# Optimization experiments

Measured on AMD Instinct MI355X. Metric: run time of the kernel, lower is better.

Reference implementation:

```python
import jax, jax.numpy as jnp
import numpy as np
from jax import lax

B, N, C_IN = 8, 16384, 32
NPOINT = 1024
RADII = (0.5, 1.0)
NSAMPLES = (16, 32)
MLPS = ((35, 32, 64), (35, 64, 128))  # first dim includes +3 for use_xyz


def setup_inputs():
    key = jax.random.key(0)
    ks = jax.random.split(key, 20)
    inp = {
        'xyz': jax.random.normal(ks[0], (B, N, 3), jnp.float32),
        'features': jax.random.normal(ks[1], (B, C_IN, N), jnp.float32),
    }
    i = 2
    for bi, spec in enumerate(MLPS):
        for li in range(len(spec) - 1):
            cin, cout = spec[li], spec[li + 1]
            inp['w%d_%d' % (bi, li)] = jax.random.normal(ks[i], (cout, cin), jnp.float32) * np.float32(1.0 / np.sqrt(cin)); i += 1
            inp['s%d_%d' % (bi, li)] = jax.random.uniform(ks[i], (cout,), jnp.float32, minval=0.5, maxval=1.5); i += 1
            inp['b%d_%d' % (bi, li)] = jax.random.normal(ks[i], (cout,), jnp.float32) * 0.1; i += 1
    return inp


def _fps(xyz, npoint):
    # iterative D-FPS, start from index 0 (matches CUDA furthest_point_sampling)
    Bb, Nn, _ = xyz.shape
    def body(carry, _):
        dists, far = carry
        centroid = jnp.take_along_axis(xyz, far[:, None, None], axis=1)  # (B,1,3)
        d = jnp.sum((xyz - centroid) ** 2, axis=-1)                       # (B,N)
        dists = jnp.minimum(dists, d)
        return (dists, jnp.argmax(dists, axis=-1).astype(jnp.int32)), far
    init = (jnp.full((Bb, Nn), 1e10, jnp.float32), jnp.zeros((Bb,), jnp.int32))
    _, idx = lax.scan(body, init, None, length=npoint)
    return idx.T  # (B, npoint)


def _ball_query(dist2, radius, nsample):
    # first-nsample-in-index-order semantics of pointnet2 ball_query;
    # empty slots padded with first hit (0 if no hit at all)
    Nn = dist2.shape[-1]
    scores = jnp.where(dist2 < radius * radius, jnp.arange(Nn, dtype=jnp.int32), Nn)
    neg, _ = lax.top_k(-scores, nsample)  # nsample smallest indices
    idx = -neg
    first = jnp.where(idx[..., :1] == Nn, 0, idx[..., :1])
    return jnp.where(idx == Nn, first, idx)


def _forward(xyz, features, params):
    fwx = jnp.concatenate([xyz.transpose(0, 2, 1), features], axis=1)   # (B,3+C,N)
    fps_idx = _fps(xyz, NPOINT)                                          # (B,P) int32
    new_xyz = jnp.take_along_axis(xyz, fps_idx[:, :, None], axis=1)      # (B,P,3)
    # pairwise squared distances via gemm (B,P,N)
    xx = jnp.sum(xyz * xyz, axis=-1)
    qq = jnp.sum(new_xyz * new_xyz, axis=-1)
    dist2 = qq[:, :, None] + xx[:, None, :] - 2.0 * jnp.einsum('bpd,bnd->bpn', new_xyz, xyz)
    centers = new_xyz.transpose(0, 2, 1)[..., None]                      # (B,3,P,1)
    outs = []
    for k in range(len(RADII)):
        idx = _ball_query(dist2, RADII[k], NSAMPLES[k])                  # (B,P,S)
        grouped = jax.vmap(lambda f, i: f[:, i])(fwx, idx)               # (B,3+C,P,S)
        x = jnp.concatenate([grouped[:, :3] - centers, grouped[:, 3:]], axis=1)
        for (w, s, b) in params[k]:
            # 1x1 Conv2d (no bias) + eval-mode BN folded into (s,b) + ReLU
            x = jax.nn.relu(jnp.einsum('oc,bcps->bops', w, x) * s[None, :, None, None] + b[None, :, None, None])
        outs.append(jnp.max(x, axis=-1))                                 # max_pool over nsample
    return new_xyz, jnp.concatenate(outs, axis=1)                        # (B,P,3), (B,192,P)


def reference(xyz, features, w0_0, s0_0, b0_0, w0_1, s0_1, b0_1, w1_0, s1_0, b1_0, w1_1, s1_1, b1_1):
    params = [[(w0_0, s0_0, b0_0), (w0_1, s0_1, b0_1)],
              [(w1_0, s1_0, b1_0), (w1_1, s1_1, b1_1)]]
    return _forward(xyz, features, params)
```

## Files before the change

kernel.cpp:

```cpp
#include <hip/hip_runtime.h>

#define B 8
#define N 16384
#define C_IN 32
#define P 1024

typedef float v2f __attribute__((ext_vector_type(2)));
typedef unsigned long long ull;

#define R8(OP) OP(0) OP(1) OP(2) OP(3) OP(4) OP(5) OP(6) OP(7)

__device__ __forceinline__ v2f pk_add(v2f a, v2f b) {
  v2f d; asm("v_pk_add_f32 %0, %1, %2" : "=v"(d) : "v"(a), "v"(b)); return d;
}
__device__ __forceinline__ v2f pk_mul(v2f a, v2f b) {
  v2f d; asm("v_pk_mul_f32 %0, %1, %2" : "=v"(d) : "v"(a), "v"(b)); return d;
}
__device__ __forceinline__ float negf(float x) {
  return __int_as_float(__float_as_int(x) ^ 0x80000000);
}

template <int CTRL>
__device__ __forceinline__ float dpp_fmax(float v) {
  float o = __int_as_float(__builtin_amdgcn_update_dpp(
      __float_as_int(v), __float_as_int(v), CTRL, 0xF, 0xF, false));
  return fmaxf(v, o);
}

__global__ __launch_bounds__(1024)
void fps_prep_kernel(const float* __restrict__ xyz,
                     const float* __restrict__ feats,
                     float* __restrict__ new_xyz,
                     float* __restrict__ ftr,
                     float* __restrict__ sox, float* __restrict__ soy,
                     float* __restrict__ soz)
{
  __shared__ __align__(16) char smem[131088];
  const int t = threadIdx.x;

  if (blockIdx.x >= 8) {
    const int pid   = blockIdx.x - 8;
    const int pb    = pid >> 6;
    const int n0    = (pid & 63) << 8;
    const float* fb = feats + (size_t)pb * (C_IN * N);
    const float* xb = xyz + (size_t)pb * (N * 3);
    float (*tile)[257] = (float(*)[257])smem;

    {
      const int c  = t >> 5;
      const int nn = (t & 31) << 3;
      const float* src = fb + (size_t)c * N + n0 + nn;
      const float4 a0 = *(const float4*)(src);
      const float4 a1 = *(const float4*)(src + 4);
      tile[c][nn + 0] = a0.x; tile[c][nn + 1] = a0.y;
      tile[c][nn + 2] = a0.z; tile[c][nn + 3] = a0.w;
      tile[c][nn + 4] = a1.x; tile[c][nn + 5] = a1.y;
      tile[c][nn + 6] = a1.z; tile[c][nn + 7] = a1.w;
    }
    if (t < 256) {
      const int n = n0 + t;
      const size_t o = (size_t)pb * N + n;
      sox[o] = xb[(size_t)n * 3 + 0];
      soy[o] = xb[(size_t)n * 3 + 1];
      soz[o] = xb[(size_t)n * 3 + 2];
    }
    __syncthreads();
    {
      const int n  = t >> 2;
      const int c0 = (t & 3) << 3;
      float4 o0, o1;
      o0.x = tile[c0 + 0][n]; o0.y = tile[c0 + 1][n];
      o0.z = tile[c0 + 2][n]; o0.w = tile[c0 + 3][n];
      o1.x = tile[c0 + 4][n]; o1.y = tile[c0 + 5][n];
      o1.z = tile[c0 + 6][n]; o1.w = tile[c0 + 7][n];
      float4* dst = (float4*)(ftr + ((size_t)pb * N + n0 + n) * 32 + c0);
      dst[0] = o0;
      dst[1] = o1;
    }
    return;
  }

  float* sx = (float*)smem;
  float* sy = sx + N;
  ull*  slot = (ull*)(smem + 2 * N * sizeof(float));

  const int b = blockIdx.x;
  const float* xb = xyz + (size_t)b * (N * 3);

  if (t == 0) { slot[0] = ~0ull; slot[1] = ~0ull; }

#define FPS_DECL(j) v2f pzp##j, dmp##j; dmp##j.x = 1e10f; dmp##j.y = 1e10f;
  R8(FPS_DECL)
#define FPS_LOADP(j) {                                                         \
    const int n0 = (t << 2) + ((j >> 1) << 12) + ((j & 1) << 1);               \
    const float2 ld0 = *(const float2*)&xb[(size_t)n0 * 3 + 0];     \
    const float2 ld1 = *(const float2*)&xb[(size_t)n0 * 3 + 2];     \
    const float2 ld2 = *(const float2*)&xb[(size_t)n0 * 3 + 4];     \
    sx[n0]     = ld0.x;  sy[n0]     = ld0.y;                                   \
    sx[n0 + 1] = ld1.y;  sy[n0 + 1] = ld2.x;                                   \
    pzp##j.x   = ld1.x;  pzp##j.y   = ld2.y;                                   \
    asm volatile("" : "+v"(pzp##j)); }
  R8(FPS_LOADP)

  float cz = xb[2];
  __syncthreads();
  float cx = sx[0], cy = sy[0];
  int sel = 0, msel = 0;

  for (int iter = 0; iter < P; ++iter) {
    msel = (t == iter) ? sel : msel;
    if (iter == P - 1) break;

    v2f cxx, cyy, czz;
    { float v = negf(cx); cxx.x = v; cxx.y = v; }
    { float v = negf(cy); cyy.x = v; cyy.y = v; }
    { float v = negf(cz); czz.x = v; czz.y = v; }

    v2f sq0, sq1, sq2, sq3, sq4, sq5, sq6, sq7;
#define FPS_XY(i, ja, jb) {                                                    \
      const int n0 = (t << 2) + ((i) << 12);                                   \
      v2f xl = *(const v2f*)&sx[n0];  v2f xh = *(const v2f*)&sx[n0 + 2];       \
      v2f yl = *(const v2f*)&sy[n0];  v2f yh = *(const v2f*)&sy[n0 + 2];       \
      v2f dxl = pk_add(xl, cxx), dyl = pk_add(yl, cyy);                        \
      v2f dxh = pk_add(xh, cxx), dyh = pk_add(yh, cyy);                        \
      sq##ja = pk_add(pk_mul(dxl, dxl), pk_mul(dyl, dyl));                     \
      sq##jb = pk_add(pk_mul(dxh, dxh), pk_mul(dyh, dyh)); }
    FPS_XY(0, 0, 1)
    FPS_XY(1, 2, 3)
    FPS_XY(2, 4, 5)
    FPS_XY(3, 6, 7)

    float bestv = -1.0f;
    int   s = 0;
#define FPS_Z(j) {                                                             \
      v2f dz = pk_add(pzp##j, czz);                                            \
      v2f dd = pk_add(sq##j, pk_mul(dz, dz));                                  \
      dmp##j.x = fminf(dmp##j.x, dd.x);                                        \
      dmp##j.y = fminf(dmp##j.y, dd.y);                                        \
      bool b0 = dmp##j.x > bestv;                                              \
      bestv = b0 ? dmp##j.x : bestv;  s = b0 ? (2 * (j))     : s;              \
      bool b1 = dmp##j.y > bestv;                                              \
      bestv = b1 ? dmp##j.y : bestv;  s = b1 ? (2 * (j) + 1) : s; }
    R8(FPS_Z)

    float wm = bestv;
    wm = dpp_fmax<0xB1>(wm);
    wm = dpp_fmax<0x4E>(wm);
    wm = dpp_fmax<0x141>(wm);
    wm = dpp_fmax<0x140>(wm);
    wm = dpp_fmax<0x142>(wm);
    wm = dpp_fmax<0x143>(wm);
    const float wmax = __int_as_float(
        __builtin_amdgcn_readlane(__float_as_int(wm), 63));

    if (bestv == wmax) {
      int nn = (t << 2) + ((s & 12) << 10) + (s & 3);
      unsigned inv = ~__float_as_uint(bestv);
      ull key = ((ull)(unsigned)(P - 1 - iter) << 46) |
                ((ull)inv << 14) | (ull)(unsigned)nn;
      atomicMin(&slot[iter & 1], key);
    }
    __syncthreads();

    ull k = slot[iter & 1];
    sel = __builtin_amdgcn_readfirstlane((int)((unsigned)k & 0x3FFFu));
    cx = sx[sel];
    cy = sy[sel];
    cz = xb[(size_t)sel * 3 + 2];
  }

  {
    const int n = msel;
    size_t o = ((size_t)b * P + t) * 3;
    new_xyz[o + 0] = sx[n];
    new_xyz[o + 1] = sy[n];
    new_xyz[o + 2] = xb[(size_t)n * 3 + 2];
  }
#undef FPS_DECL
#undef FPS_LOADP
#undef FPS_XY
#undef FPS_Z
}

__global__ __launch_bounds__(256) void ballq_kernel(
    const float* __restrict__ sox, const float* __restrict__ soy,
    const float* __restrict__ soz, const float* __restrict__ new_xyz,
    int* __restrict__ idx0, int* __restrict__ idx1)
{
  const int wid  = blockIdx.x * 4 + (threadIdx.x >> 6);
  const int lane = threadIdx.x & 63;
  const int b = wid >> 10;
  const int p = wid & (P - 1);
  const float* X = sox + (size_t)b * N;
  const float* Y = soy + (size_t)b * N;
  const float* Z = soz + (size_t)b * N;
  const size_t bp = (size_t)b * P + p;
  const float cx = new_xyz[bp * 3 + 0];
  const float cy = new_xyz[bp * 3 + 1];
  const float cz = new_xyz[bp * 3 + 2];
  const float qv = __fadd_rn(__fadd_rn(__fmul_rn(cx, cx), __fmul_rn(cy, cy)),
                             __fmul_rn(cz, cz));
  int* __restrict__ o0 = idx0 + bp * 16;
  int* __restrict__ o1 = idx1 + bp * 32;

  int c0 = 0, c1 = 0, f0 = 0, f1 = 0;
  const ull below = (1ull << lane) - 1ull;

  for (int base = 0; base < N; base += 256) {
    const int n0 = base + (lane << 2);
    const float4 xv = *(const float4*)&X[n0];
    const float4 yv = *(const float4*)&Y[n0];
    const float4 zv = *(const float4*)&Z[n0];

    float d2[4];
#pragma unroll
    for (int e = 0; e < 4; ++e) {
      const float x = (e == 0) ? xv.x : (e == 1) ? xv.y : (e == 2) ? xv.z : xv.w;
      const float y = (e == 0) ? yv.x : (e == 1) ? yv.y : (e == 2) ? yv.z : yv.w;
      const float z = (e == 0) ? zv.x : (e == 1) ? zv.y : (e == 2) ? zv.z : zv.w;
      const float xx = __fadd_rn(__fadd_rn(__fmul_rn(x, x), __fmul_rn(y, y)),
                                 __fmul_rn(z, z));
      const float dot = __fadd_rn(__fadd_rn(__fmul_rn(cx, x), __fmul_rn(cy, y)),
                                  __fmul_rn(cz, z));
      d2[e] = __fsub_rn(__fadd_rn(qv, xx), __fmul_rn(2.0f, dot));
    }

    ull m0[4], m1[4];
#pragma unroll
    for (int e = 0; e < 4; ++e) {
      m0[e] = __ballot(d2[e] < 0.25f);
      m1[e] = __ballot(d2[e] < 1.0f);
    }

#define BQ_PROC(m, cap, oarr, cnt, fst) {                                      \
    const int tot = (int)(__builtin_popcountll(m[0]) +                         \
                          __builtin_popcountll(m[1]) +                         \
                          __builtin_popcountll(m[2]) +                         \
                          __builtin_popcountll(m[3]));                         \
    if (cnt < cap && tot) {                                                    \
      if (cnt == 0) {                                                          \
        const ull any = m[0] | m[1] | m[2] | m[3];                             \
        const int lm = __builtin_ctzll(any);                                   \
        const int em = ((m[0] >> lm) & 1ull) ? 0 :                             \
                       ((m[1] >> lm) & 1ull) ? 1 :                             \
                       ((m[2] >> lm) & 1ull) ? 2 : 3;                          \
        fst = base + (lm << 2) + em;                                           \
      }                                                                        \
      int pos = cnt + (int)(__builtin_popcountll(m[0] & below) +               \
                            __builtin_popcountll(m[1] & below) +               \
                            __builtin_popcountll(m[2] & below) +               \
                            __builtin_popcountll(m[3] & below));               \
      const bool h0 = (m[0] >> lane) & 1ull;                                   \
      const bool h1 = (m[1] >> lane) & 1ull;                                   \
      const bool h2 = (m[2] >> lane) & 1ull;                                   \
      const bool h3 = (m[3] >> lane) & 1ull;                                   \
      if (h0 && pos < cap) oarr[pos] = n0 + 0;                                 \
      pos += h0;                                                               \
      if (h1 && pos < cap) oarr[pos] = n0 + 1;                                 \
      pos += h1;                                                               \
      if (h2 && pos < cap) oarr[pos] = n0 + 2;                                 \
      pos += h2;                                                               \
      if (h3 && pos < cap) oarr[pos] = n0 + 3;                                 \
    }                                                                          \
    cnt = min(cap, cnt + tot); }

    BQ_PROC(m0, 16, o0, c0, f0)
    BQ_PROC(m1, 32, o1, c1, f1)
#undef BQ_PROC
    if (c0 >= 16 && c1 >= 32) break;
  }
  for (int s = c0 + lane; s < 16; s += 64) o0[s] = f0;
  for (int s = c1 + lane; s < 32; s += 64) o1[s] = f1;
}

template <int S, int C1, int C2, int CH_OFF>
__global__ __launch_bounds__(256) void mlp_kernel(
    const float* __restrict__ xyz, const float* __restrict__ ftr,
    const float* __restrict__ new_xyz, const int* __restrict__ idx,
    const float* __restrict__ w1, const float* __restrict__ s1,
    const float* __restrict__ b1, const float* __restrict__ w2,
    const float* __restrict__ s2, const float* __restrict__ b2,
    float* __restrict__ out)
{
  static_assert((C1 * S) % 512 == 0 && (C2 * S) % 512 == 0, "mapping");
  __shared__ float wl1[35][C1];
  __shared__ float wl2[C1][C2 + 1];
  __shared__ float sb1[2][C1];
  __shared__ float sb2[2][C2];
  __shared__ float xs[35][S];
  __shared__ float o1s[C1][S];
  __shared__ float pm[256];

  const int tid = threadIdx.x;
  for (int i = tid; i < 35 * C1; i += 256) {
    int o = i % C1, c = i / C1;
    wl1[c][o] = w1[o * 35 + c];
  }
  for (int i = tid; i < (C1 * C2) / 4; i += 256) {
    const float4 v = *(const float4*)&w2[i * 4];
    const int o = (i * 4) / C1, c = (i * 4) % C1;
    wl2[c + 0][o] = v.x; wl2[c + 1][o] = v.y;
    wl2[c + 2][o] = v.z; wl2[c + 3][o] = v.w;
  }
  if (tid < C1) { sb1[0][tid] = s1[tid]; sb1[1][tid] = b1[tid]; }
  if (tid < C2) { sb2[0][tid] = s2[tid]; sb2[1][tid] = b2[tid]; }

  const int b  = blockIdx.x / (P / 8);
  const int p0 = (blockIdx.x % (P / 8)) * 8;
  const float* xb = xyz + (size_t)b * (N * 3);
  const float* fb = ftr + (size_t)b * N * 32;
  __syncthreads();

  for (int pi = 0; pi < 8; ++pi) {
    const int p = p0 + pi;
    const size_t bp = (size_t)b * P + p;
    const int* ip = idx + bp * S;
    const float cx = new_xyz[bp * 3 + 0];
    const float cy = new_xyz[bp * 3 + 1];
    const float cz = new_xyz[bp * 3 + 2];
    for (int s2i = tid; s2i < S; s2i += 256) {
      const int n = ip[s2i];
      xs[0][s2i] = xb[n * 3 + 0] - cx;
      xs[1][s2i] = xb[n * 3 + 1] - cy;
      xs[2][s2i] = xb[n * 3 + 2] - cz;
    }
    for (int i = tid; i < S * 8; i += 256) {
      const int s = i >> 3, q = i & 7;
      const int n = ip[s];
      const float4 v = *(const float4*)&fb[(size_t)n * 32 + q * 4];
      const int c = 3 + q * 4;
      xs[c + 0][s] = v.x; xs[c + 1][s] = v.y;
      xs[c + 2][s] = v.z; xs[c + 3][s] = v.w;
    }
    __syncthreads();
    {
      constexpr int OPT  = (C1 * S) / 256;
      constexpr int OPT2 = OPT / 2;
      const int s  = tid % S;
      const int ob = (tid / S) * OPT;
      v2f acc[OPT2];
#pragma unroll
      for (int m = 0; m < OPT2; ++m) { acc[m].x = 0.0f; acc[m].y = 0.0f; }
      for (int c = 0; c < 35; ++c) {
        const float xv = xs[c][s];
        v2f xv2; xv2.x = xv; xv2.y = xv;
#pragma unroll
        for (int m = 0; m < OPT2; ++m) {
          const v2f w = *(const v2f*)&wl1[c][ob + 2 * m];
          asm("v_pk_fma_f32 %0, %1, %2, %0"
              : "+v"(acc[m]) : "v"(xv2), "v"(w));
        }
      }
#pragma unroll
      for (int m = 0; m < OPT2; ++m) {
        const int o0i = ob + 2 * m, o1i = ob + 2 * m + 1;
        float v0 = fmaf(acc[m].x, sb1[0][o0i], sb1[1][o0i]);
        float v1 = fmaf(acc[m].y, sb1[0][o1i], sb1[1][o1i]);
        o1s[o0i][s] = fmaxf(v0, 0.0f);
        o1s[o1i][s] = fmaxf(v1, 0.0f);
      }
    }
    __syncthreads();
    {
      constexpr int NS  = (C2 * S) / 256;
      constexpr int NS2 = NS / 2;
      const int o2 = tid % C2;
      const int sb = (tid / C2) * NS;
      v2f acc[NS2];
#pragma unroll
      for (int m = 0; m < NS2; ++m) { acc[m].x = 0.0f; acc[m].y = 0.0f; }
      for (int c = 0; c < C1; ++c) {
        const float wv = wl2[c][o2];
        v2f wv2; wv2.x = wv; wv2.y = wv;
#pragma unroll
        for (int m = 0; m < NS2; ++m) {
          const v2f ov = *(const v2f*)&o1s[c][sb + 2 * m];
          asm("v_pk_fma_f32 %0, %1, %2, %0"
              : "+v"(acc[m]) : "v"(wv2), "v"(ov));
        }
      }
      const float scale = sb2[0][o2], bias = sb2[1][o2];
      float m2 = 0.0f;
#pragma unroll
      for (int m = 0; m < NS2; ++m) {
        m2 = fmaxf(m2, fmaf(acc[m].x, scale, bias));
        m2 = fmaxf(m2, fmaf(acc[m].y, scale, bias));
      }
      pm[tid] = m2;
      __syncthreads();
      if (tid < C2) {
        float mm = pm[tid];
#pragma unroll
        for (int g = 1; g < 256 / C2; ++g) mm = fmaxf(mm, pm[tid + g * C2]);
        out[((size_t)b * 192 + CH_OFF + tid) * P + p] = mm;
      }
    }
    __syncthreads();
  }
}

extern "C" void kernel_launch(void* const* d_in, const int* in_sizes, int n_in,
                              void* d_out, int out_size, void* d_ws, size_t ws_size,
                              hipStream_t stream) {
  const float* xyz   = (const float*)d_in[0];
  const float* feats = (const float*)d_in[1];
  const float* w0_0 = (const float*)d_in[2];
  const float* s0_0 = (const float*)d_in[3];
  const float* b0_0 = (const float*)d_in[4];
  const float* w0_1 = (const float*)d_in[5];
  const float* s0_1 = (const float*)d_in[6];
  const float* b0_1 = (const float*)d_in[7];
  const float* w1_0 = (const float*)d_in[8];
  const float* s1_0 = (const float*)d_in[9];
  const float* b1_0 = (const float*)d_in[10];
  const float* w1_1 = (const float*)d_in[11];
  const float* s1_1 = (const float*)d_in[12];
  const float* b1_1 = (const float*)d_in[13];

  float* out      = (float*)d_out;
  float* new_xyz  = out;
  float* feat_out = out + (size_t)B * P * 3;

  char* w = (char*)d_ws;
  float* ftr = (float*)w; w += (size_t)B * N * 32 * sizeof(float);
  float* sox = (float*)w; w += (size_t)B * N * sizeof(float);
  float* soy = (float*)w; w += (size_t)B * N * sizeof(float);
  float* soz = (float*)w; w += (size_t)B * N * sizeof(float);
  int* idx0 = (int*)w; w += (size_t)B * P * 16 * sizeof(int);
  int* idx1 = (int*)w; w += (size_t)B * P * 32 * sizeof(int);

  fps_prep_kernel<<<dim3(8 + B * (N / 256)), dim3(1024), 0, stream>>>(
      xyz, feats, new_xyz, ftr, sox, soy, soz);
  ballq_kernel<<<dim3(B * P / 4), dim3(256), 0, stream>>>(
      sox, soy, soz, new_xyz, idx0, idx1);
  mlp_kernel<16, 32, 64, 0><<<dim3(B * P / 8), dim3(256), 0, stream>>>(
      xyz, ftr, new_xyz, idx0, w0_0, s0_0, b0_0, w0_1, s0_1, b0_1, feat_out);
  mlp_kernel<32, 64, 128, 64><<<dim3(B * P / 8), dim3(256), 0, stream>>>(
      xyz, ftr, new_xyz, idx1, w1_0, s1_0, b1_0, w1_1, s1_1, b1_1, feat_out);
}
```

Before: 2.193 ms.

## Fuse ball query and both MLP branches into one per-wave kernel

```diff
diff --git a/kernel.cpp b/kernel.cpp
--- a/kernel.cpp
+++ b/kernel.cpp
@@ -8,7 +8,7 @@
 typedef float v2f __attribute__((ext_vector_type(2)));
 typedef unsigned long long ull;
 
-#define R8(OP) OP(0) OP(1) OP(2) OP(3) OP(4) OP(5) OP(6) OP(7)
+#define R8M(OP) OP(0) OP(1) OP(2) OP(3) OP(4) OP(5) OP(6) OP(7)
 
 __device__ __forceinline__ v2f pk_add(v2f a, v2f b) {
   v2f d; asm("v_pk_add_f32 %0, %1, %2" : "=v"(d) : "v"(a), "v"(b)); return d;
@@ -19,7 +19,6 @@
 __device__ __forceinline__ float negf(float x) {
   return __int_as_float(__float_as_int(x) ^ 0x80000000);
 }
-
 template <int CTRL>
 __device__ __forceinline__ float dpp_fmax(float v) {
   float o = __int_as_float(__builtin_amdgcn_update_dpp(
@@ -90,17 +89,17 @@
   if (t == 0) { slot[0] = ~0ull; slot[1] = ~0ull; }
 
 #define FPS_DECL(j) v2f pzp##j, dmp##j; dmp##j.x = 1e10f; dmp##j.y = 1e10f;
-  R8(FPS_DECL)
+  R8M(FPS_DECL)
 #define FPS_LOADP(j) {                                                         \
     const int n0 = (t << 2) + ((j >> 1) << 12) + ((j & 1) << 1);               \
-    const float2 ld0 = *(const float2*)&xb[(size_t)n0 * 3 + 0];     \
-    const float2 ld1 = *(const float2*)&xb[(size_t)n0 * 3 + 2];     \
-    const float2 ld2 = *(const float2*)&xb[(size_t)n0 * 3 + 4];     \
+    const float2 ld0 = *(const float2*)&xb[(size_t)n0 * 3 + 0];                \
+    const float2 ld1 = *(const float2*)&xb[(size_t)n0 * 3 + 2];                \
+    const float2 ld2 = *(const float2*)&xb[(size_t)n0 * 3 + 4];                \
     sx[n0]     = ld0.x;  sy[n0]     = ld0.y;                                   \
     sx[n0 + 1] = ld1.y;  sy[n0 + 1] = ld2.x;                                   \
     pzp##j.x   = ld1.x;  pzp##j.y   = ld2.y;                                   \
     asm volatile("" : "+v"(pzp##j)); }
-  R8(FPS_LOADP)
+  R8M(FPS_LOADP)
 
   float cz = xb[2];
   __syncthreads();
@@ -141,7 +140,7 @@
       bestv = b0 ? dmp##j.x : bestv;  s = b0 ? (2 * (j))     : s;              \
       bool b1 = dmp##j.y > bestv;                                              \
       bestv = b1 ? dmp##j.y : bestv;  s = b1 ? (2 * (j) + 1) : s; }
-    R8(FPS_Z)
+    R8M(FPS_Z)
 
     float wm = bestv;
     wm = dpp_fmax<0xB1>(wm);
@@ -182,221 +181,249 @@
 #undef FPS_Z
 }
 
-__global__ __launch_bounds__(256) void ballq_kernel(
-    const float* __restrict__ sox, const float* __restrict__ soy,
-    const float* __restrict__ soz, const float* __restrict__ new_xyz,
-    int* __restrict__ idx0, int* __restrict__ idx1)
+#define OFF_W10 0
+#define OFF_W20 4480
+#define OFF_W11 12672
+#define OFF_W21 21632
+#define OFF_SB  54400
+#define OFF_PW  56704
+#define PW_SZ   12864
+
+template <int S, int C1, int C2>
+__device__ void wave_mlp(const int lane, const int* __restrict__ ip,
+                         const float* __restrict__ xb,
+                         const float* __restrict__ fb,
+                         const float cx, const float cy, const float cz,
+                         const float* __restrict__ wl1,
+                         const float* __restrict__ wl2,
+                         const float* __restrict__ s1v,
+                         const float* __restrict__ b1v,
+                         const float* __restrict__ s2v,
+                         const float* __restrict__ b2v,
+                         float* __restrict__ xs, float* __restrict__ o1s,
+                         float* __restrict__ outp)
 {
-  const int wid  = blockIdx.x * 4 + (threadIdx.x >> 6);
-  const int lane = threadIdx.x & 63;
-  const int b = wid >> 10;
-  const int p = wid & (P - 1);
-  const float* X = sox + (size_t)b * N;
-  const float* Y = soy + (size_t)b * N;
-  const float* Z = soz + (size_t)b * N;
-  const size_t bp = (size_t)b * P + p;
+  for (int s = lane; s < S; s += 64) {
+    const int n = ip[s];
+    xs[0 * S + s] = xb[n * 3 + 0] - cx;
+    xs[1 * S + s] = xb[n * 3 + 1] - cy;
+    xs[2 * S + s] = xb[n * 3 + 2] - cz;
+  }
+  for (int i = lane; i < S * 8; i += 64) {
+    const int s = i >> 3, q = i & 7;
+    const int n = ip[s];
+    const float4 v = *(const float4*)&fb[(size_t)n * 32 + q * 4];
+    const int c = 3 + q * 4;
+    xs[(c + 0) * S + s] = v.x; xs[(c + 1) * S + s] = v.y;
+    xs[(c + 2) * S + s] = v.z; xs[(c + 3) * S + s] = v.w;
+  }
+  {
+    const int s   = lane % S;
+    const int grp = lane / S;
+    constexpr int OPL = (C1 * S) / 64;
+    constexpr int NP  = (OPL < 8) ? OPL : 8;
+    const int ob0 = grp * OPL;
+#pragma unroll
+    for (int pass = 0; pass < OPL / NP; ++pass) {
+      const int ob = ob0 + pass * NP;
+      float acc[NP];
+#pragma unroll
+      for (int j = 0; j < NP; ++j) acc[j] = 0.0f;
+      for (int c = 0; c < 35; ++c) {
+        const float xv = xs[c * S + s];
+#pragma unroll
+        for (int j4 = 0; j4 < NP / 4; ++j4) {
+          const float4 w4 = *(const float4*)&wl1[c * C1 + ob + 4 * j4];
+          acc[4 * j4 + 0] = fmaf(xv, w4.x, acc[4 * j4 + 0]);
+          acc[4 * j4 + 1] = fmaf(xv, w4.y, acc[4 * j4 + 1]);
+          acc[4 * j4 + 2] = fmaf(xv, w4.z, acc[4 * j4 + 2]);
+          acc[4 * j4 + 3] = fmaf(xv, w4.w, acc[4 * j4 + 3]);
+        }
+      }
+#pragma unroll
+      for (int j = 0; j < NP; ++j) {
+        const int o = ob + j;
+        o1s[o * S + s] = fmaxf(fmaf(acc[j], s1v[o], b1v[o]), 0.0f);
+      }
+    }
+  }
+  {
+#pragma unroll
+    for (int k = 0; k < C2 / 64; ++k) {
+      const int o2 = lane + 64 * k;
+      const float sc = s2v[o2], bi = b2v[o2];
+      float m = 0.0f;
+#pragma unroll
+      for (int sb0 = 0; sb0 < S / 16; ++sb0) {
+        float acc[16];
+#pragma unroll
+        for (int j = 0; j < 16; ++j) acc[j] = 0.0f;
+        for (int c = 0; c < C1; ++c) {
+          const float wv = wl2[c * C2 + o2];
+#pragma unroll
+          for (int j4 = 0; j4 < 4; ++j4) {
+            const float4 ov = *(const float4*)&o1s[c * S + sb0 * 16 + 4 * j4];
+            acc[4 * j4 + 0] = fmaf(ov.x, wv, acc[4 * j4 + 0]);
+            acc[4 * j4 + 1] = fmaf(ov.y, wv, acc[4 * j4 + 1]);
+            acc[4 * j4 + 2] = fmaf(ov.z, wv, acc[4 * j4 + 2]);
+            acc[4 * j4 + 3] = fmaf(ov.w, wv, acc[4 * j4 + 3]);
+          }
+        }
+#pragma unroll
+        for (int j = 0; j < 16; ++j) m = fmaxf(m, fmaf(acc[j], sc, bi));
+      }
+      outp[(size_t)o2 * P] = m;
+    }
+  }
+}
+
+__global__ __launch_bounds__(256)
+void fused_kernel(const float* __restrict__ xyz,
+                  const float* __restrict__ ftr,
+                  const float* __restrict__ sox, const float* __restrict__ soy,
+                  const float* __restrict__ soz,
+                  const float* __restrict__ new_xyz,
+                  const float* __restrict__ w00, const float* __restrict__ s00,
+                  const float* __restrict__ b00, const float* __restrict__ w01,
+                  const float* __restrict__ s01, const float* __restrict__ b01,
+                  const float* __restrict__ w10, const float* __restrict__ s10,
+                  const float* __restrict__ b10, const float* __restrict__ w11,
+                  const float* __restrict__ s11, const float* __restrict__ b11,
+                  float* __restrict__ feat_out)
+{
+  __shared__ __align__(16) char smem[108160];
+  const int t = threadIdx.x;
+
+  float* W10 = (float*)(smem + OFF_W10);
+  float* W20 = (float*)(smem + OFF_W20);
+  float* W11 = (float*)(smem + OFF_W11);
+  float* W21 = (float*)(smem + OFF_W21);
+  float* SBv = (float*)(smem + OFF_SB);
+  float* SB10s = SBv;        float* SB10b = SBv + 32;
+  float* SB20s = SBv + 64;   float* SB20b = SBv + 128;
+  float* SB11s = SBv + 192;  float* SB11b = SBv + 256;
+  float* SB21s = SBv + 320;  float* SB21b = SBv + 448;
+
+  for (int i = t; i < 35 * 32; i += 256) {
+    const int o = i % 32, c = i / 32;
+    W10[c * 32 + o] = w00[o * 35 + c];
+  }
+  for (int i = t; i < 32 * 64; i += 256) {
+    const int c = i >> 6, o = i & 63;
+    W20[c * 64 + o] = w01[o * 32 + c];
+  }
+  for (int i = t; i < 35 * 64; i += 256) {
+    const int o = i % 64, c = i / 64;
+    W11[c * 64 + o] = w10[o * 35 + c];
+  }
+  for (int i = t; i < 64 * 128; i += 256) {
+    const int c = i >> 7, o = i & 127;
+    W21[c * 128 + o] = w11[o * 64 + c];
+  }
+  if (t < 32)  { SB10s[t] = s00[t]; SB10b[t] = b00[t]; }
+  if (t < 64)  { SB20s[t] = s01[t]; SB20b[t] = b01[t];
+                 SB11s[t] = s10[t]; SB11b[t] = b10[t]; }
+  if (t < 128) { SB21s[t] = s11[t]; SB21b[t] = b11[t]; }
+  __syncthreads();
+
+  const int wv   = t >> 6;
+  const int lane = t & 63;
+  const int wid  = blockIdx.x * 4 + wv;
+  const int bb = wid >> 10;
+  const int p  = wid & (P - 1);
+
+  int*   widx0 = (int*)(smem + OFF_PW + wv * PW_SZ);
+  int*   widx1 = widx0 + 16;
+  float* wxs   = (float*)(smem + OFF_PW + wv * PW_SZ + 192);
+  float* wo1   = wxs + 35 * 32;
+
+  const size_t bp = (size_t)bb * P + p;
   const float cx = new_xyz[bp * 3 + 0];
   const float cy = new_xyz[bp * 3 + 1];
   const float cz = new_xyz[bp * 3 + 2];
-  const float qv = __fadd_rn(__fadd_rn(__fmul_rn(cx, cx), __fmul_rn(cy, cy)),
-                             __fmul_rn(cz, cz));
-  int* __restrict__ o0 = idx0 + bp * 16;
-  int* __restrict__ o1 = idx1 + bp * 32;
-
-  int c0 = 0, c1 = 0, f0 = 0, f1 = 0;
-  const ull below = (1ull << lane) - 1ull;
-
-  for (int base = 0; base < N; base += 256) {
-    const int n0 = base + (lane << 2);
-    const float4 xv = *(const float4*)&X[n0];
-    const float4 yv = *(const float4*)&Y[n0];
-    const float4 zv = *(const float4*)&Z[n0];
-
-    float d2[4];
-#pragma unroll
-    for (int e = 0; e < 4; ++e) {
-      const float x = (e == 0) ? xv.x : (e == 1) ? xv.y : (e == 2) ? xv.z : xv.w;
-      const float y = (e == 0) ? yv.x : (e == 1) ? yv.y : (e == 2) ? yv.z : yv.w;
-      const float z = (e == 0) ? zv.x : (e == 1) ? zv.y : (e == 2) ? zv.z : zv.w;
-      const float xx = __fadd_rn(__fadd_rn(__fmul_rn(x, x), __fmul_rn(y, y)),
-                                 __fmul_rn(z, z));
-      const float dot = __fadd_rn(__fadd_rn(__fmul_rn(cx, x), __fmul_rn(cy, y)),
-                                  __fmul_rn(cz, z));
-      d2[e] = __fsub_rn(__fadd_rn(qv, xx), __fmul_rn(2.0f, dot));
-    }
-
-    ull m0[4], m1[4];
-#pragma unroll
-    for (int e = 0; e < 4; ++e) {
-      m0[e] = __ballot(d2[e] < 0.25f);
-      m1[e] = __ballot(d2[e] < 1.0f);
-    }
-
+
+  {
+    const float* X = sox + (size_t)bb * N;
+    const float* Y = soy + (size_t)bb * N;
+    const float* Z = soz + (size_t)bb * N;
+    const float qv = __fadd_rn(__fadd_rn(__fmul_rn(cx, cx), __fmul_rn(cy, cy)),
+                               __fmul_rn(cz, cz));
+    int c0 = 0, c1 = 0, f0 = 0, f1 = 0;
+    const ull below = (1ull << lane) - 1ull;
+
+    for (int base = 0; base < N; base += 256) {
+      const int n0 = base + (lane << 2);
+      const float4 xv = *(const float4*)&X[n0];
+      const float4 yv = *(const float4*)&Y[n0];
+      const float4 zv = *(const float4*)&Z[n0];
+      float d2[4];
+#pragma unroll
+      for (int e = 0; e < 4; ++e) {
+        const float x = (e == 0) ? xv.x : (e == 1) ? xv.y : (e == 2) ? xv.z : xv.w;
+        const float y = (e == 0) ? yv.x : (e == 1) ? yv.y : (e == 2) ? yv.z : yv.w;
+        const float z = (e == 0) ? zv.x : (e == 1) ? zv.y : (e == 2) ? zv.z : zv.w;
+        const float xx = __fadd_rn(__fadd_rn(__fmul_rn(x, x), __fmul_rn(y, y)),
+                                   __fmul_rn(z, z));
+        const float dot = __fadd_rn(__fadd_rn(__fmul_rn(cx, x), __fmul_rn(cy, y)),
+                                    __fmul_rn(cz, z));
+        d2[e] = __fsub_rn(__fadd_rn(qv, xx), __fmul_rn(2.0f, dot));
+      }
+      ull m0[4], m1[4];
+#pragma unroll
+      for (int e = 0; e < 4; ++e) {
+        m0[e] = __ballot(d2[e] < 0.25f);
+        m1[e] = __ballot(d2[e] < 1.0f);
+      }
 #define BQ_PROC(m, cap, oarr, cnt, fst) {                                      \
-    const int tot = (int)(__builtin_popcountll(m[0]) +                         \
-                          __builtin_popcountll(m[1]) +                         \
-                          __builtin_popcountll(m[2]) +                         \
-                          __builtin_popcountll(m[3]));                         \
-    if (cnt < cap && tot) {                                                    \
-      if (cnt == 0) {                                                          \
-        const ull any = m[0] | m[1] | m[2] | m[3];                             \
-        const int lm = __builtin_ctzll(any);                                   \
-        const int em = ((m[0] >> lm) & 1ull) ? 0 :                             \
-                       ((m[1] >> lm) & 1ull) ? 1 :                             \
-                       ((m[2] >> lm) & 1ull) ? 2 : 3;                          \
-        fst = base + (lm << 2) + em;                                           \
+      const int tot = (int)(__builtin_popcountll(m[0]) +                       \
+                            __builtin_popcountll(m[1]) +                       \
+                            __builtin_popcountll(m[2]) +                       \
+                            __builtin_popcountll(m[3]));                       \
+      if (cnt < cap && tot) {                                                  \
+        if (cnt == 0) {                                                        \
+          const ull any = m[0] | m[1] | m[2] | m[3];                           \
+          const int lm = __builtin_ctzll(any);                                 \
+          const int em = ((m[0] >> lm) & 1ull) ? 0 :                           \
+                         ((m[1] >> lm) & 1ull) ? 1 :                           \
+                         ((m[2] >> lm) & 1ull) ? 2 : 3;                        \
+          fst = base + (lm << 2) + em;                                         \
+        }                                                                      \
+        int pos = cnt + (int)(__builtin_popcountll(m[0] & below) +             \
+                              __builtin_popcountll(m[1] & below) +             \
+                              __builtin_popcountll(m[2] & below) +             \
+                              __builtin_popcountll(m[3] & below));             \
+        const bool h0 = (m[0] >> lane) & 1ull;                                 \
+        const bool h1 = (m[1] >> lane) & 1ull;                                 \
+        const bool h2 = (m[2] >> lane) & 1ull;                                 \
+        const bool h3 = (m[3] >> lane) & 1ull;                                 \
+        if (h0 && pos < cap) oarr[pos] = n0 + 0;                               \
+        pos += h0;                                                             \
+        if (h1 && pos < cap) oarr[pos] = n0 + 1;                               \
+        pos += h1;                                                             \
+        if (h2 && pos < cap) oarr[pos] = n0 + 2;                               \
+        pos += h2;                                                             \
+        if (h3 && pos < cap) oarr[pos] = n0 + 3;                               \
       }                                                                        \
-      int pos = cnt + (int)(__builtin_popcountll(m[0] & below) +               \
-                            __builtin_popcountll(m[1] & below) +               \
-                            __builtin_popcountll(m[2] & below) +               \
-                            __builtin_popcountll(m[3] & below));               \
-      const bool h0 = (m[0] >> lane) & 1ull;                                   \
-      const bool h1 = (m[1] >> lane) & 1ull;                                   \
-      const bool h2 = (m[2] >> lane) & 1ull;                                   \
-      const bool h3 = (m[3] >> lane) & 1ull;                                   \
-      if (h0 && pos < cap) oarr[pos] = n0 + 0;                                 \
-      pos += h0;                                                               \
-      if (h1 && pos < cap) oarr[pos] = n0 + 1;                                 \
-      pos += h1;                                                               \
-      if (h2 && pos < cap) oarr[pos] = n0 + 2;                                 \
-      pos += h2;                                                               \
-      if (h3 && pos < cap) oarr[pos] = n0 + 3;                                 \
-    }                                                                          \
-    cnt = min(cap, cnt + tot); }
-
-    BQ_PROC(m0, 16, o0, c0, f0)
-    BQ_PROC(m1, 32, o1, c1, f1)
+      cnt = min(cap, cnt + tot); }
+      BQ_PROC(m0, 16, widx0, c0, f0)
+      BQ_PROC(m1, 32, widx1, c1, f1)
 #undef BQ_PROC
-    if (c0 >= 16 && c1 >= 32) break;
-  }
-  for (int s = c0 + lane; s < 16; s += 64) o0[s] = f0;
-  for (int s = c1 + lane; s < 32; s += 64) o1[s] = f1;
-}
-
-template <int S, int C1, int C2, int CH_OFF>
-__global__ __launch_bounds__(256) void mlp_kernel(
-    const float* __restrict__ xyz, const float* __restrict__ ftr,
-    const float* __restrict__ new_xyz, const int* __restrict__ idx,
-    const float* __restrict__ w1, const float* __restrict__ s1,
-    const float* __restrict__ b1, const float* __restrict__ w2,
-    const float* __restrict__ s2, const float* __restrict__ b2,
-    float* __restrict__ out)
-{
-  static_assert((C1 * S) % 512 == 0 && (C2 * S) % 512 == 0, "mapping");
-  __shared__ float wl1[35][C1];
-  __shared__ float wl2[C1][C2 + 1];
-  __shared__ float sb1[2][C1];
-  __shared__ float sb2[2][C2];
-  __shared__ float xs[35][S];
-  __shared__ float o1s[C1][S];
-  __shared__ float pm[256];
-
-  const int tid = threadIdx.x;
-  for (int i = tid; i < 35 * C1; i += 256) {
-    int o = i % C1, c = i / C1;
-    wl1[c][o] = w1[o * 35 + c];
-  }
-  for (int i = tid; i < (C1 * C2) / 4; i += 256) {
-    const float4 v = *(const float4*)&w2[i * 4];
-    const int o = (i * 4) / C1, c = (i * 4) % C1;
-    wl2[c + 0][o] = v.x; wl2[c + 1][o] = v.y;
-    wl2[c + 2][o] = v.z; wl2[c + 3][o] = v.w;
-  }
-  if (tid < C1) { sb1[0][tid] = s1[tid]; sb1[1][tid] = b1[tid]; }
-  if (tid < C2) { sb2[0][tid] = s2[tid]; sb2[1][tid] = b2[tid]; }
-
-  const int b  = blockIdx.x / (P / 8);
-  const int p0 = (blockIdx.x % (P / 8)) * 8;
-  const float* xb = xyz + (size_t)b * (N * 3);
-  const float* fb = ftr + (size_t)b * N * 32;
-  __syncthreads();
-
-  for (int pi = 0; pi < 8; ++pi) {
-    const int p = p0 + pi;
-    const size_t bp = (size_t)b * P + p;
-    const int* ip = idx + bp * S;
-    const float cx = new_xyz[bp * 3 + 0];
-    const float cy = new_xyz[bp * 3 + 1];
-    const float cz = new_xyz[bp * 3 + 2];
-    for (int s2i = tid; s2i < S; s2i += 256) {
-      const int n = ip[s2i];
-      xs[0][s2i] = xb[n * 3 + 0] - cx;
-      xs[1][s2i] = xb[n * 3 + 1] - cy;
-      xs[2][s2i] = xb[n * 3 + 2] - cz;
-    }
-    for (int i = tid; i < S * 8; i += 256) {
-      const int s = i >> 3, q = i & 7;
-      const int n = ip[s];
-      const float4 v = *(const float4*)&fb[(size_t)n * 32 + q * 4];
-      const int c = 3 + q * 4;
-      xs[c + 0][s] = v.x; xs[c + 1][s] = v.y;
-      xs[c + 2][s] = v.z; xs[c + 3][s] = v.w;
-    }
-    __syncthreads();
-    {
-      constexpr int OPT  = (C1 * S) / 256;
-      constexpr int OPT2 = OPT / 2;
-      const int s  = tid % S;
-      const int ob = (tid / S) * OPT;
-      v2f acc[OPT2];
-#pragma unroll
-      for (int m = 0; m < OPT2; ++m) { acc[m].x = 0.0f; acc[m].y = 0.0f; }
-      for (int c = 0; c < 35; ++c) {
-        const float xv = xs[c][s];
-        v2f xv2; xv2.x = xv; xv2.y = xv;
-#pragma unroll
-        for (int m = 0; m < OPT2; ++m) {
-          const v2f w = *(const v2f*)&wl1[c][ob + 2 * m];
-          asm("v_pk_fma_f32 %0, %1, %2, %0"
-              : "+v"(acc[m]) : "v"(xv2), "v"(w));
-        }
-      }
-#pragma unroll
-      for (int m = 0; m < OPT2; ++m) {
-        const int o0i = ob + 2 * m, o1i = ob + 2 * m + 1;
-        float v0 = fmaf(acc[m].x, sb1[0][o0i], sb1[1][o0i]);
-        float v1 = fmaf(acc[m].y, sb1[0][o1i], sb1[1][o1i]);
-        o1s[o0i][s] = fmaxf(v0, 0.0f);
-        o1s[o1i][s] = fmaxf(v1, 0.0f);
-      }
-    }
-    __syncthreads();
-    {
-      constexpr int NS  = (C2 * S) / 256;
-      constexpr int NS2 = NS / 2;
-      const int o2 = tid % C2;
-      const int sb = (tid / C2) * NS;
-      v2f acc[NS2];
-#pragma unroll
-      for (int m = 0; m < NS2; ++m) { acc[m].x = 0.0f; acc[m].y = 0.0f; }
-      for (int c = 0; c < C1; ++c) {
-        const float wv = wl2[c][o2];
-        v2f wv2; wv2.x = wv; wv2.y = wv;
-#pragma unroll
-        for (int m = 0; m < NS2; ++m) {
-          const v2f ov = *(const v2f*)&o1s[c][sb + 2 * m];
-          asm("v_pk_fma_f32 %0, %1, %2, %0"
-              : "+v"(acc[m]) : "v"(wv2), "v"(ov));
-        }
-      }
-      const float scale = sb2[0][o2], bias = sb2[1][o2];
-      float m2 = 0.0f;
-#pragma unroll
-      for (int m = 0; m < NS2; ++m) {
-        m2 = fmaxf(m2, fmaf(acc[m].x, scale, bias));
-        m2 = fmaxf(m2, fmaf(acc[m].y, scale, bias));
-      }
-      pm[tid] = m2;
-      __syncthreads();
-      if (tid < C2) {
-        float mm = pm[tid];
-#pragma unroll
-        for (int g = 1; g < 256 / C2; ++g) mm = fmaxf(mm, pm[tid + g * C2]);
-        out[((size_t)b * 192 + CH_OFF + tid) * P + p] = mm;
-      }
-    }
-    __syncthreads();
-  }
+      if (c0 >= 16 && c1 >= 32) break;
+    }
+    for (int s = c0 + lane; s < 16; s += 64) widx0[s] = f0;
+    for (int s = c1 + lane; s < 32; s += 64) widx1[s] = f1;
+  }
+
+  const float* xb2 = xyz + (size_t)bb * (N * 3);
+  const float* fb2 = ftr + (size_t)bb * N * 32;
+  float* outp0 = feat_out + ((size_t)bb * 192 + 0) * P + p;
+  float* outp1 = feat_out + ((size_t)bb * 192 + 64) * P + p;
+  wave_mlp<16, 32, 64>(lane, widx0, xb2, fb2, cx, cy, cz,
+                       W10, W20, SB10s, SB10b, SB20s, SB20b,
+                       wxs, wo1, outp0);
+  wave_mlp<32, 64, 128>(lane, widx1, xb2, fb2, cx, cy, cz,
+                        W11, W21, SB11s, SB11b, SB21s, SB21b,
+                        wxs, wo1, outp1);
 }
 
 extern "C" void kernel_launch(void* const* d_in, const int* in_sizes, int n_in,
@@ -426,15 +453,11 @@
   float* sox = (float*)w; w += (size_t)B * N * sizeof(float);
   float* soy = (float*)w; w += (size_t)B * N * sizeof(float);
   float* soz = (float*)w; w += (size_t)B * N * sizeof(float);
-  int* idx0 = (int*)w; w += (size_t)B * P * 16 * sizeof(int);
-  int* idx1 = (int*)w; w += (size_t)B * P * 32 * sizeof(int);
 
   fps_prep_kernel<<<dim3(8 + B * (N / 256)), dim3(1024), 0, stream>>>(
       xyz, feats, new_xyz, ftr, sox, soy, soz);
-  ballq_kernel<<<dim3(B * P / 4), dim3(256), 0, stream>>>(
-      sox, soy, soz, new_xyz, idx0, idx1);
-  mlp_kernel<16, 32, 64, 0><<<dim3(B * P / 8), dim3(256), 0, stream>>>(
-      xyz, ftr, new_xyz, idx0, w0_0, s0_0, b0_0, w0_1, s0_1, b0_1, feat_out);
-  mlp_kernel<32, 64, 128, 64><<<dim3(B * P / 8), dim3(256), 0, stream>>>(
-      xyz, ftr, new_xyz, idx1, w1_0, s1_0, b1_0, w1_1, s1_1, b1_1, feat_out);
-}
+  fused_kernel<<<dim3(B * P / 4), dim3(256), 0, stream>>>(
+      xyz, ftr, sox, soy, soz, new_xyz,
+      w0_0, s0_0, b0_0, w0_1, s0_1, b0_1,
+      w1_0, s1_0, b1_0, w1_1, s1_1, b1_1, feat_out);
+}
```

Result: slower. 2.363 ms (+7.8%).
